# Performance work log

Measured on AMD Instinct MI355X. Metric: run time of the kernel, lower is better.

## Reference

```python
import jax, jax.numpy as jnp
import numpy as np

T, H, I, E = 8192, 1024, 2816, 8


def setup_inputs() -> dict:
    key = jax.random.key(0)
    ks = jax.random.split(key, 4)
    x = jax.random.normal(ks[0], (T, H), dtype=jnp.float32)
    router_logits = jax.random.normal(ks[1], (T, E), dtype=jnp.float32)
    # params scaled like trained weights
    w13 = jax.random.normal(ks[2], (E, 2 * I, H), dtype=jnp.float32) * (1.0 / np.sqrt(H))
    w2 = jax.random.normal(ks[3], (E, H, I), dtype=jnp.float32) * (1.0 / np.sqrt(I))
    return {"x": x, "router_logits": router_logits, "w13": w13, "w2": w2, "top_k": 2}


def reference(x, router_logits, w13, w2, top_k):
    """select_experts (softmax scoring, top-k, renormalize) + fused_experts (SiLU-gated MLP per expert, weighted combine)."""
    Ttok, Hd = x.shape
    Ex, twoI, _ = w13.shape
    Id = twoI // 2
    # --- router: softmax -> top_k -> renormalize ---
    probs = jax.nn.softmax(router_logits.astype(jnp.float32), axis=-1)  # [T, E]
    topk_w, topk_ids = jax.lax.top_k(probs, top_k)                      # [T, k]
    topk_w = topk_w / jnp.sum(topk_w, axis=-1, keepdims=True)
    # per-expert combine weight matrix [T, E] (scatter of topk weights)
    comb = jnp.zeros((Ttok, Ex), dtype=x.dtype).at[
        jnp.arange(Ttok)[:, None], topk_ids
    ].add(topk_w.astype(x.dtype))
    # --- expert MLPs: out = sum_e comb[:,e] * (silu(x W1_e^T) * (x W3_e^T)) W2_e^T ---
    out = jnp.zeros_like(x)
    for e in range(Ex):  # small fixed expert count
        gate = x @ w13[e, :Id].T          # [T, I]
        up = x @ w13[e, Id:].T            # [T, I]
        h = jax.nn.silu(gate) * up        # [T, I]
        out = out + comb[:, e:e + 1] * (h @ w2[e].T)  # [T, H]
    return out
```

## Files before the change

kernel.cpp:

```cpp
#include <hip/hip_runtime.h>
#include <hip/hip_bf16.h>

#define T_TOK 8192
#define H_DIM 1024
#define I_DIM 2816
#define E_NUM 8
#define R_TOT (2 * T_TOK)

typedef __hip_bfloat16 bf16;
typedef __attribute__((ext_vector_type(8))) short short8;
typedef __attribute__((ext_vector_type(4))) float floatx4;

__device__ inline unsigned short f2b(float f) {
    bf16 b = __float2bfloat16(f);
    unsigned short u;
    __builtin_memcpy(&u, &b, 2);
    return u;
}

__device__ inline short8 ld_cvt8(const float* p) {
    float4 f0 = *(const float4*)p;
    float4 f1 = *(const float4*)(p + 4);
    short8 r;
    r[0] = (short)f2b(f0.x); r[1] = (short)f2b(f0.y);
    r[2] = (short)f2b(f0.z); r[3] = (short)f2b(f0.w);
    r[4] = (short)f2b(f1.x); r[5] = (short)f2b(f1.y);
    r[6] = (short)f2b(f1.z); r[7] = (short)f2b(f1.w);
    return r;
}

__device__ inline void gl_lds16(const void* g, void* l) {
    __builtin_amdgcn_global_load_lds(
        (const __attribute__((address_space(1))) void*)g,
        (__attribute__((address_space(3))) void*)l, 16, 0, 0);
}


__global__ __launch_bounds__(256) void cvt_bf16_kernel(const float* __restrict__ in,
                                                       bf16* __restrict__ out, int n8) {
    int stride = gridDim.x * blockDim.x;
    for (int i = blockIdx.x * blockDim.x + threadIdx.x; i < n8; i += stride) {
        short8 v = ld_cvt8(in + (size_t)i * 8);
        *(short8*)(out + (size_t)i * 8) = v;
    }
}


__global__ void zero_counts_kernel(int* counts) {
    if (threadIdx.x < E_NUM) counts[threadIdx.x] = 0;
}

__global__ void zero_out_kernel(float* __restrict__ out) {
    size_t i = ((size_t)blockIdx.x * 256 + threadIdx.x) * 4;
    float4 z = {0.0f, 0.0f, 0.0f, 0.0f};
    *(float4*)(out + i) = z;
}

__global__ void router_kernel(const float* __restrict__ logits,
                              int* __restrict__ topk_id,
                              float* __restrict__ topk_w,
                              int* __restrict__ counts) {
    int t = blockIdx.x * blockDim.x + threadIdx.x;
    if (t >= T_TOK) return;
    float l[E_NUM];
#pragma unroll
    for (int e = 0; e < E_NUM; e++) l[e] = logits[t * E_NUM + e];
    int i0 = 0;
#pragma unroll
    for (int e = 1; e < E_NUM; e++)
        if (l[e] > l[i0]) i0 = e;
    int i1 = (i0 == 0) ? 1 : 0;
#pragma unroll
    for (int e = 0; e < E_NUM; e++) {
        if (e == i0 || e == i1) continue;
        if (l[e] > l[i1]) i1 = e;
    }
    float p1 = __expf(l[i1] - l[i0]);
    float w0 = 1.0f / (1.0f + p1);
    float w1 = p1 / (1.0f + p1);
    topk_id[2 * t] = i0;
    topk_id[2 * t + 1] = i1;
    topk_w[2 * t] = w0;
    topk_w[2 * t + 1] = w1;
    atomicAdd(&counts[i0], 1);
    atomicAdd(&counts[i1], 1);
}

__global__ void offsets_kernel(const int* __restrict__ counts,
                               int* __restrict__ offs,
                               int* __restrict__ cursor) {
    if (threadIdx.x == 0 && blockIdx.x == 0) {
        int acc = 0;
        for (int e = 0; e < E_NUM; e++) {
            offs[e] = acc;
            cursor[e] = acc;
            acc += counts[e];
        }
        offs[E_NUM] = acc;
    }
}

__global__ void scatter_kernel(const int* __restrict__ topk_id,
                               const float* __restrict__ topk_w,
                               int* __restrict__ cursor,
                               int* __restrict__ rowtok,
                               float* __restrict__ wrow) {
    int t = blockIdx.x * blockDim.x + threadIdx.x;
    if (t >= T_TOK) return;
#pragma unroll
    for (int j = 0; j < 2; j++) {
        int e = topk_id[2 * t + j];
        int r = atomicAdd(&cursor[e], 1);
        rowtok[r] = t;
        wrow[r] = topk_w[2 * t + j];
    }
}


__global__ __launch_bounds__(256) void gemm1_bf16_kernel(
    const bf16* __restrict__ xb, const bf16* __restrict__ wptr,
    long long wstride, int e_base,
    const int* __restrict__ offs, const int* __restrict__ rowtok,
    bf16* __restrict__ h) {
    const int ei = blockIdx.y >> 6;
    const int e = e_base + ei;
    const int tm = blockIdx.y & 63;
    const int mBeg = offs[e], mEnd = offs[e + 1];
    const int m0 = mBeg + tm * 128;
    if (m0 >= mEnd) return;
    const int n0 = blockIdx.x * 128;

    __shared__ alignas(16) bf16 As[128 * 32];
    __shared__ alignas(16) bf16 Bg[128 * 32];
    __shared__ alignas(16) bf16 Bu[128 * 32];

    const int tid = threadIdx.x;
    const int lane = tid & 63;
    const int wv = tid >> 6;
    const int wr = wv >> 1, wc = wv & 1;

    const int c0 = tid, c1 = tid + 256;
    const int ar0 = c0 >> 2, ks0 = (c0 & 3) * 8;
    const int ar1 = c1 >> 2, ks1 = (c1 & 3) * 8;
    const bf16* aG0 = xb + (size_t)rowtok[min(m0 + ar0, R_TOT - 1)] * H_DIM + ks0;
    const bf16* aG1 = xb + (size_t)rowtok[min(m0 + ar1, R_TOT - 1)] * H_DIM + ks1;
    const bf16* w13e = wptr + (size_t)ei * wstride;
    const bf16* bG0 = w13e + (size_t)(n0 + ar0) * H_DIM + ks0;
    const bf16* bG1 = w13e + (size_t)(n0 + ar1) * H_DIM + ks1;
    const bf16* uG0 = w13e + (size_t)(I_DIM + n0 + ar0) * H_DIM + ks0;
    const bf16* uG1 = w13e + (size_t)(I_DIM + n0 + ar1) * H_DIM + ks1;

    const int wb = wv * 64;
    bf16* dA0 = As + (size_t)wb * 8;
    bf16* dA1 = As + (size_t)(wb + 256) * 8;
    bf16* dG0 = Bg + (size_t)wb * 8;
    bf16* dG1 = Bg + (size_t)(wb + 256) * 8;
    bf16* dU0 = Bu + (size_t)wb * 8;
    bf16* dU1 = Bu + (size_t)(wb + 256) * 8;

    floatx4 accG[4][4] = {};
    floatx4 accU[4][4] = {};

    const int lr = lane & 15;
    const int kg = lane >> 4;

    for (int kt = 0; kt < H_DIM; kt += 32) {
        gl_lds16(aG0 + kt, dA0);
        gl_lds16(aG1 + kt, dA1);
        gl_lds16(bG0 + kt, dG0);
        gl_lds16(bG1 + kt, dG1);
        gl_lds16(uG0 + kt, dU0);
        gl_lds16(uG1 + kt, dU1);
        __syncthreads();

        short8 af[4], bgf[4], buf2[4];
#pragma unroll
        for (int i = 0; i < 4; i++)
            af[i] = *(const short8*)(As + (wr * 64 + i * 16 + lr) * 32 + kg * 8);
#pragma unroll
        for (int j = 0; j < 4; j++) {
            bgf[j] = *(const short8*)(Bg + (wc * 64 + j * 16 + lr) * 32 + kg * 8);
            buf2[j] = *(const short8*)(Bu + (wc * 64 + j * 16 + lr) * 32 + kg * 8);
        }
#pragma unroll
        for (int i = 0; i < 4; i++)
#pragma unroll
            for (int j = 0; j < 4; j++) {
                accG[i][j] = __builtin_amdgcn_mfma_f32_16x16x32_bf16(af[i], bgf[j], accG[i][j], 0, 0, 0);
                accU[i][j] = __builtin_amdgcn_mfma_f32_16x16x32_bf16(af[i], buf2[j], accU[i][j], 0, 0, 0);
            }
        __syncthreads();
    }

    const int quad = lane >> 4;
#pragma unroll
    for (int i = 0; i < 4; i++) {
        const int grb = m0 + wr * 64 + i * 16 + quad * 4;
#pragma unroll
        for (int j = 0; j < 4; j++) {
            const int gc = n0 + wc * 64 + j * 16 + lr;
#pragma unroll
            for (int v = 0; v < 4; v++) {
                const int gr = grb + v;
                if (gr < mEnd) {
                    float g = accG[i][j][v];
                    float u = accU[i][j][v];
                    float s = g / (1.0f + __expf(-g));
                    h[(size_t)gr * I_DIM + gc] = __float2bfloat16(s * u);
                }
            }
        }
    }
}


__global__ __launch_bounds__(256) void gemm2_bf16_kernel(
    const bf16* __restrict__ hbuf, const bf16* __restrict__ wptr,
    long long wstride, int e_base,
    const int* __restrict__ offs, const int* __restrict__ rowtok,
    const float* __restrict__ wrow, float* __restrict__ out) {
    const int ei = blockIdx.y >> 6;
    const int e = e_base + ei;
    const int tm = blockIdx.y & 63;
    const int mBeg = offs[e], mEnd = offs[e + 1];
    const int m0 = mBeg + tm * 128;
    if (m0 >= mEnd) return;
    const int n0 = blockIdx.x * 128;

    __shared__ alignas(16) bf16 As[128 * 32];
    __shared__ alignas(16) bf16 Bs[128 * 32];

    const int tid = threadIdx.x;
    const int lane = tid & 63;
    const int wv = tid >> 6;
    const int wr = wv >> 1, wc = wv & 1;

    const int c0 = tid, c1 = tid + 256;
    const int ar0 = c0 >> 2, ks0 = (c0 & 3) * 8;
    const int ar1 = c1 >> 2, ks1 = (c1 & 3) * 8;
    const bf16* aG0 = hbuf + (size_t)min(m0 + ar0, R_TOT - 1) * I_DIM + ks0;
    const bf16* aG1 = hbuf + (size_t)min(m0 + ar1, R_TOT - 1) * I_DIM + ks1;
    const bf16* w2e = wptr + (size_t)ei * wstride;
    const bf16* bG0 = w2e + (size_t)(n0 + ar0) * I_DIM + ks0;
    const bf16* bG1 = w2e + (size_t)(n0 + ar1) * I_DIM + ks1;

    const int wb = wv * 64;
    bf16* dA0 = As + (size_t)wb * 8;
    bf16* dA1 = As + (size_t)(wb + 256) * 8;
    bf16* dB0 = Bs + (size_t)wb * 8;
    bf16* dB1 = Bs + (size_t)(wb + 256) * 8;

    floatx4 acc[4][4] = {};
    const int lr = lane & 15;
    const int kg = lane >> 4;

    for (int kt = 0; kt < I_DIM; kt += 32) {
        gl_lds16(aG0 + kt, dA0);
        gl_lds16(aG1 + kt, dA1);
        gl_lds16(bG0 + kt, dB0);
        gl_lds16(bG1 + kt, dB1);
        __syncthreads();

        short8 af[4], bf_[4];
#pragma unroll
        for (int i = 0; i < 4; i++)
            af[i] = *(const short8*)(As + (wr * 64 + i * 16 + lr) * 32 + kg * 8);
#pragma unroll
        for (int j = 0; j < 4; j++)
            bf_[j] = *(const short8*)(Bs + (wc * 64 + j * 16 + lr) * 32 + kg * 8);
#pragma unroll
        for (int i = 0; i < 4; i++)
#pragma unroll
            for (int j = 0; j < 4; j++)
                acc[i][j] = __builtin_amdgcn_mfma_f32_16x16x32_bf16(af[i], bf_[j], acc[i][j], 0, 0, 0);
        __syncthreads();
    }

    const int quad = lane >> 4;
#pragma unroll
    for (int i = 0; i < 4; i++) {
        const int grb = m0 + wr * 64 + i * 16 + quad * 4;
#pragma unroll
        for (int j = 0; j < 4; j++) {
            const int gc = n0 + wc * 64 + j * 16 + lr;
#pragma unroll
            for (int v = 0; v < 4; v++) {
                const int gr = grb + v;
                if (gr < mEnd) {
                    const int t = rowtok[gr];
                    atomicAdd(&out[(size_t)t * H_DIM + gc], wrow[gr] * acc[i][j][v]);
                }
            }
        }
    }
}


__global__ __launch_bounds__(256) void gemm1_f32_kernel(
    const float* __restrict__ x, const float* __restrict__ w13,
    const int* __restrict__ offs, const int* __restrict__ rowtok,
    bf16* __restrict__ h) {
    const int e = blockIdx.y >> 6;
    const int tm = blockIdx.y & 63;
    const int mBeg = offs[e], mEnd = offs[e + 1];
    const int m0 = mBeg + tm * 128;
    if (m0 >= mEnd) return;
    const int n0 = blockIdx.x * 128;

    __shared__ alignas(16) bf16 As[128 * 32];
    __shared__ alignas(16) bf16 Bg[128 * 32];
    __shared__ alignas(16) bf16 Bu[128 * 32];

    const int tid = threadIdx.x;
    const int lane = tid & 63;
    const int wv = tid >> 6;
    const int wr = wv >> 1, wc = wv & 1;

    const int c0 = tid, c1 = tid + 256;
    const int ar0 = c0 >> 2, ks0 = (c0 & 3) * 8;
    const int ar1 = c1 >> 2, ks1 = (c1 & 3) * 8;
    const int rr0 = min(m0 + ar0, R_TOT - 1);
    const int rr1 = min(m0 + ar1, R_TOT - 1);
    const float* aG0 = x + (size_t)rowtok[rr0] * H_DIM + ks0;
    const float* aG1 = x + (size_t)rowtok[rr1] * H_DIM + ks1;
    const float* w13e = w13 + (size_t)e * (2 * I_DIM) * H_DIM;
    const float* bG0 = w13e + (size_t)(n0 + ar0) * H_DIM + ks0;
    const float* bG1 = w13e + (size_t)(n0 + ar1) * H_DIM + ks1;
    const float* uG0 = w13e + (size_t)(I_DIM + n0 + ar0) * H_DIM + ks0;
    const float* uG1 = w13e + (size_t)(I_DIM + n0 + ar1) * H_DIM + ks1;

    floatx4 accG[4][4] = {};
    floatx4 accU[4][4] = {};

    const int lr = lane & 15;
    const int kg = lane >> 4;

    for (int kt = 0; kt < H_DIM; kt += 32) {
        short8 va0 = ld_cvt8(aG0 + kt);
        short8 va1 = ld_cvt8(aG1 + kt);
        short8 vg0 = ld_cvt8(bG0 + kt);
        short8 vg1 = ld_cvt8(bG1 + kt);
        short8 vu0 = ld_cvt8(uG0 + kt);
        short8 vu1 = ld_cvt8(uG1 + kt);
        __syncthreads();
        *(short8*)(As + c0 * 8) = va0;
        *(short8*)(As + c1 * 8) = va1;
        *(short8*)(Bg + c0 * 8) = vg0;
        *(short8*)(Bg + c1 * 8) = vg1;
        *(short8*)(Bu + c0 * 8) = vu0;
        *(short8*)(Bu + c1 * 8) = vu1;
        __syncthreads();

        short8 af[4], bgf[4], buf2[4];
#pragma unroll
        for (int i = 0; i < 4; i++)
            af[i] = *(const short8*)(As + (wr * 64 + i * 16 + lr) * 32 + kg * 8);
#pragma unroll
        for (int j = 0; j < 4; j++) {
            bgf[j] = *(const short8*)(Bg + (wc * 64 + j * 16 + lr) * 32 + kg * 8);
            buf2[j] = *(const short8*)(Bu + (wc * 64 + j * 16 + lr) * 32 + kg * 8);
        }
#pragma unroll
        for (int i = 0; i < 4; i++)
#pragma unroll
            for (int j = 0; j < 4; j++) {
                accG[i][j] = __builtin_amdgcn_mfma_f32_16x16x32_bf16(af[i], bgf[j], accG[i][j], 0, 0, 0);
                accU[i][j] = __builtin_amdgcn_mfma_f32_16x16x32_bf16(af[i], buf2[j], accU[i][j], 0, 0, 0);
            }
    }

    const int quad = lane >> 4;
#pragma unroll
    for (int i = 0; i < 4; i++) {
        const int grb = m0 + wr * 64 + i * 16 + quad * 4;
#pragma unroll
        for (int j = 0; j < 4; j++) {
            const int gc = n0 + wc * 64 + j * 16 + lr;
#pragma unroll
            for (int v = 0; v < 4; v++) {
                const int gr = grb + v;
                if (gr < mEnd) {
                    float g = accG[i][j][v];
                    float u = accU[i][j][v];
                    float s = g / (1.0f + __expf(-g));
                    h[(size_t)gr * I_DIM + gc] = __float2bfloat16(s * u);
                }
            }
        }
    }
}

__global__ __launch_bounds__(256) void gemm2_f32_kernel(
    const bf16* __restrict__ hbuf, const float* __restrict__ w2,
    const int* __restrict__ offs, const int* __restrict__ rowtok,
    const float* __restrict__ wrow, float* __restrict__ out) {
    const int e = blockIdx.y >> 6;
    const int tm = blockIdx.y & 63;
    const int mBeg = offs[e], mEnd = offs[e + 1];
    const int m0 = mBeg + tm * 128;
    if (m0 >= mEnd) return;
    const int n0 = blockIdx.x * 128;

    __shared__ alignas(16) bf16 As[128 * 32];
    __shared__ alignas(16) bf16 Bs[128 * 32];

    const int tid = threadIdx.x;
    const int lane = tid & 63;
    const int wv = tid >> 6;
    const int wr = wv >> 1, wc = wv & 1;

    const int c0 = tid, c1 = tid + 256;
    const int ar0 = c0 >> 2, ks0 = (c0 & 3) * 8;
    const int ar1 = c1 >> 2, ks1 = (c1 & 3) * 8;
    const bf16* aG0 = hbuf + (size_t)min(m0 + ar0, R_TOT - 1) * I_DIM + ks0;
    const bf16* aG1 = hbuf + (size_t)min(m0 + ar1, R_TOT - 1) * I_DIM + ks1;
    const float* w2e = w2 + (size_t)e * H_DIM * I_DIM;
    const float* bG0 = w2e + (size_t)(n0 + ar0) * I_DIM + ks0;
    const float* bG1 = w2e + (size_t)(n0 + ar1) * I_DIM + ks1;

    floatx4 acc[4][4] = {};
    const int lr = lane & 15;
    const int kg = lane >> 4;

    for (int kt = 0; kt < I_DIM; kt += 32) {
        short8 va0 = *(const short8*)(aG0 + kt);
        short8 va1 = *(const short8*)(aG1 + kt);
        short8 vb0 = ld_cvt8(bG0 + kt);
        short8 vb1 = ld_cvt8(bG1 + kt);
        __syncthreads();
        *(short8*)(As + c0 * 8) = va0;
        *(short8*)(As + c1 * 8) = va1;
        *(short8*)(Bs + c0 * 8) = vb0;
        *(short8*)(Bs + c1 * 8) = vb1;
        __syncthreads();

        short8 af[4], bf_[4];
#pragma unroll
        for (int i = 0; i < 4; i++)
            af[i] = *(const short8*)(As + (wr * 64 + i * 16 + lr) * 32 + kg * 8);
#pragma unroll
        for (int j = 0; j < 4; j++)
            bf_[j] = *(const short8*)(Bs + (wc * 64 + j * 16 + lr) * 32 + kg * 8);
#pragma unroll
        for (int i = 0; i < 4; i++)
#pragma unroll
            for (int j = 0; j < 4; j++)
                acc[i][j] = __builtin_amdgcn_mfma_f32_16x16x32_bf16(af[i], bf_[j], acc[i][j], 0, 0, 0);
    }

    const int quad = lane >> 4;
#pragma unroll
    for (int i = 0; i < 4; i++) {
        const int grb = m0 + wr * 64 + i * 16 + quad * 4;
#pragma unroll
        for (int j = 0; j < 4; j++) {
            const int gc = n0 + wc * 64 + j * 16 + lr;
#pragma unroll
            for (int v = 0; v < 4; v++) {
                const int gr = grb + v;
                if (gr < mEnd) {
                    const int t = rowtok[gr];
                    atomicAdd(&out[(size_t)t * H_DIM + gc], wrow[gr] * acc[i][j][v]);
                }
            }
        }
    }
}


extern "C" void kernel_launch(void* const* d_in, const int* in_sizes, int n_in,
                              void* d_out, int out_size, void* d_ws, size_t ws_size,
                              hipStream_t stream) {
    const float* x = (const float*)d_in[0];
    const float* rl = (const float*)d_in[1];
    const float* w13 = (const float*)d_in[2];
    const float* w2 = (const float*)d_in[3];
    float* out = (float*)d_out;

    char* ws = (char*)d_ws;
    int* counts = (int*)(ws);
    int* offs = (int*)(ws + 256);
    int* cursor = (int*)(ws + 512);
    int* topk_id = (int*)(ws + 1024);
    float* topk_w = (float*)(ws + 1024 + 65536);
    int* rowtok = (int*)(ws + 1024 + 2 * 65536);
    float* wrow = (float*)(ws + 1024 + 3 * 65536);

    const size_t BASE = 1024 + 4 * 65536;
    const size_t H_BYTES = (size_t)R_TOT * I_DIM * 2;
    const size_t XB_BYTES = (size_t)T_TOK * H_DIM * 2;
    const size_t W13_BYTES = (size_t)E_NUM * 2 * I_DIM * H_DIM * 2;
    const size_t W13_SLICE = (size_t)2 * I_DIM * H_DIM * 2;
    const size_t W2_SLICE = (size_t)H_DIM * I_DIM * 2;

    bf16* h = (bf16*)(ws + BASE);
    bf16* xb = (bf16*)(ws + BASE + H_BYTES);
    bf16* wbuf = (bf16*)(ws + BASE + H_BYTES + XB_BYTES);

    const size_t NEED_BULK = BASE + H_BYTES + XB_BYTES + W13_BYTES;
    const size_t NEED_SLICE = BASE + H_BYTES + XB_BYTES + W13_SLICE;

    zero_out_kernel<<<(T_TOK * H_DIM) / (256 * 4), 256, 0, stream>>>(out);
    zero_counts_kernel<<<1, 64, 0, stream>>>(counts);
    router_kernel<<<(T_TOK + 255) / 256, 256, 0, stream>>>(rl, topk_id, topk_w, counts);
    offsets_kernel<<<1, 64, 0, stream>>>(counts, offs, cursor);
    scatter_kernel<<<(T_TOK + 255) / 256, 256, 0, stream>>>(topk_id, topk_w, cursor, rowtok, wrow);

    if (ws_size >= NEED_BULK) {
        cvt_bf16_kernel<<<2048, 256, 0, stream>>>(x, xb, (T_TOK * H_DIM) / 8);
        cvt_bf16_kernel<<<2048, 256, 0, stream>>>(w13, wbuf, (int)(W13_BYTES / 2 / 8));
        gemm1_bf16_kernel<<<dim3(I_DIM / 128, E_NUM * 64), 256, 0, stream>>>(
            xb, wbuf, (long long)2 * I_DIM * H_DIM, 0, offs, rowtok, h);
        cvt_bf16_kernel<<<2048, 256, 0, stream>>>(w2, wbuf, (E_NUM * H_DIM * I_DIM) / 8);
        gemm2_bf16_kernel<<<dim3(H_DIM / 128, E_NUM * 64), 256, 0, stream>>>(
            h, wbuf, (long long)H_DIM * I_DIM, 0, offs, rowtok, wrow, out);
    } else if (ws_size >= NEED_SLICE) {
        cvt_bf16_kernel<<<2048, 256, 0, stream>>>(x, xb, (T_TOK * H_DIM) / 8);
        for (int e = 0; e < E_NUM; e++) {
            cvt_bf16_kernel<<<1024, 256, 0, stream>>>(
                w13 + (size_t)e * 2 * I_DIM * H_DIM, wbuf, (int)(W13_SLICE / 2 / 8));
            gemm1_bf16_kernel<<<dim3(I_DIM / 128, 64), 256, 0, stream>>>(
                xb, wbuf, 0LL, e, offs, rowtok, h);
        }
        for (int e = 0; e < E_NUM; e++) {
            cvt_bf16_kernel<<<1024, 256, 0, stream>>>(
                w2 + (size_t)e * H_DIM * I_DIM, wbuf, (int)(W2_SLICE / 2 / 8));
            gemm2_bf16_kernel<<<dim3(H_DIM / 128, 64), 256, 0, stream>>>(
                h, wbuf, 0LL, e, offs, rowtok, wrow, out);
        }
    } else {
        gemm1_f32_kernel<<<dim3(I_DIM / 128, E_NUM * 64), 256, 0, stream>>>(
            x, w13, offs, rowtok, h);
        gemm2_f32_kernel<<<dim3(H_DIM / 128, E_NUM * 64), 256, 0, stream>>>(
            h, w2, offs, rowtok, wrow, out);
    }
}
```

Measured before the change: 1.184 ms.

## Double-buffer LDS tiles in both expert GEMMs to overlap loads with MFMA

Both grouped GEMM kernels now keep two LDS buffers per operand and prefetch the next K tile with direct global-to-LDS loads while MFMAs run on the current tile. This drops one barrier per iteration and is meant to hide global memory latency. Launch bounds also request three blocks per CU. The extra LDS (48 KB for gemm1) and the occupancy hint may limit residency or force register spills. Correctness relies on the barrier at the end of each iteration also covering completion of the async LDS writes.

Result: slower. 1.846 ms (+55.9%).

```diff
diff --git a/kernel.cpp b/kernel.cpp
--- a/kernel.cpp
+++ b/kernel.cpp
@@ -117,7 +117,7 @@
 }
 
 
-__global__ __launch_bounds__(256) void gemm1_bf16_kernel(
+__global__ __launch_bounds__(256, 3) void gemm1_bf16_kernel(
     const bf16* __restrict__ xb, const bf16* __restrict__ wptr,
     long long wstride, int e_base,
     const int* __restrict__ offs, const int* __restrict__ rowtok,
@@ -130,9 +130,9 @@
     if (m0 >= mEnd) return;
     const int n0 = blockIdx.x * 128;
 
-    __shared__ alignas(16) bf16 As[128 * 32];
-    __shared__ alignas(16) bf16 Bg[128 * 32];
-    __shared__ alignas(16) bf16 Bu[128 * 32];
+    __shared__ alignas(16) bf16 As[2][128 * 32];
+    __shared__ alignas(16) bf16 Bg[2][128 * 32];
+    __shared__ alignas(16) bf16 Bu[2][128 * 32];
 
     const int tid = threadIdx.x;
     const int lane = tid & 63;
@@ -150,13 +150,16 @@
     const bf16* uG0 = w13e + (size_t)(I_DIM + n0 + ar0) * H_DIM + ks0;
     const bf16* uG1 = w13e + (size_t)(I_DIM + n0 + ar1) * H_DIM + ks1;
 
-    const int wb = wv * 64;
-    bf16* dA0 = As + (size_t)wb * 8;
-    bf16* dA1 = As + (size_t)(wb + 256) * 8;
-    bf16* dG0 = Bg + (size_t)wb * 8;
-    bf16* dG1 = Bg + (size_t)(wb + 256) * 8;
-    bf16* dU0 = Bu + (size_t)wb * 8;
-    bf16* dU1 = Bu + (size_t)(wb + 256) * 8;
+    const int wb8 = (wv * 64) * 8;
+    const int wb8b = (wv * 64 + 256) * 8;
+
+#define STG1(B, KT)                          \
+    gl_lds16(aG0 + (KT), &As[B][wb8]);       \
+    gl_lds16(aG1 + (KT), &As[B][wb8b]);      \
+    gl_lds16(bG0 + (KT), &Bg[B][wb8]);       \
+    gl_lds16(bG1 + (KT), &Bg[B][wb8b]);      \
+    gl_lds16(uG0 + (KT), &Bu[B][wb8]);       \
+    gl_lds16(uG1 + (KT), &Bu[B][wb8b]);
 
     floatx4 accG[4][4] = {};
     floatx4 accU[4][4] = {};
@@ -164,23 +167,21 @@
     const int lr = lane & 15;
     const int kg = lane >> 4;
 
+    STG1(0, 0);
+    __syncthreads();
+
+    int cur = 0;
     for (int kt = 0; kt < H_DIM; kt += 32) {
-        gl_lds16(aG0 + kt, dA0);
-        gl_lds16(aG1 + kt, dA1);
-        gl_lds16(bG0 + kt, dG0);
-        gl_lds16(bG1 + kt, dG1);
-        gl_lds16(uG0 + kt, dU0);
-        gl_lds16(uG1 + kt, dU1);
-        __syncthreads();
+        if (kt + 32 < H_DIM) { STG1(cur ^ 1, kt + 32); }
 
         short8 af[4], bgf[4], buf2[4];
 #pragma unroll
         for (int i = 0; i < 4; i++)
-            af[i] = *(const short8*)(As + (wr * 64 + i * 16 + lr) * 32 + kg * 8);
+            af[i] = *(const short8*)(&As[cur][(wr * 64 + i * 16 + lr) * 32 + kg * 8]);
 #pragma unroll
         for (int j = 0; j < 4; j++) {
-            bgf[j] = *(const short8*)(Bg + (wc * 64 + j * 16 + lr) * 32 + kg * 8);
-            buf2[j] = *(const short8*)(Bu + (wc * 64 + j * 16 + lr) * 32 + kg * 8);
+            bgf[j] = *(const short8*)(&Bg[cur][(wc * 64 + j * 16 + lr) * 32 + kg * 8]);
+            buf2[j] = *(const short8*)(&Bu[cur][(wc * 64 + j * 16 + lr) * 32 + kg * 8]);
         }
 #pragma unroll
         for (int i = 0; i < 4; i++)
@@ -190,7 +191,9 @@
                 accU[i][j] = __builtin_amdgcn_mfma_f32_16x16x32_bf16(af[i], buf2[j], accU[i][j], 0, 0, 0);
             }
         __syncthreads();
-    }
+        cur ^= 1;
+    }
+#undef STG1
 
     const int quad = lane >> 4;
 #pragma unroll
@@ -214,7 +217,7 @@
 }
 
 
-__global__ __launch_bounds__(256) void gemm2_bf16_kernel(
+__global__ __launch_bounds__(256, 3) void gemm2_bf16_kernel(
     const bf16* __restrict__ hbuf, const bf16* __restrict__ wptr,
     long long wstride, int e_base,
     const int* __restrict__ offs, const int* __restrict__ rowtok,
@@ -227,8 +230,8 @@
     if (m0 >= mEnd) return;
     const int n0 = blockIdx.x * 128;
 
-    __shared__ alignas(16) bf16 As[128 * 32];
-    __shared__ alignas(16) bf16 Bs[128 * 32];
+    __shared__ alignas(16) bf16 As[2][128 * 32];
+    __shared__ alignas(16) bf16 Bs[2][128 * 32];
 
     const int tid = threadIdx.x;
     const int lane = tid & 63;
@@ -244,37 +247,42 @@
     const bf16* bG0 = w2e + (size_t)(n0 + ar0) * I_DIM + ks0;
     const bf16* bG1 = w2e + (size_t)(n0 + ar1) * I_DIM + ks1;
 
-    const int wb = wv * 64;
-    bf16* dA0 = As + (size_t)wb * 8;
-    bf16* dA1 = As + (size_t)(wb + 256) * 8;
-    bf16* dB0 = Bs + (size_t)wb * 8;
-    bf16* dB1 = Bs + (size_t)(wb + 256) * 8;
+    const int wb8 = (wv * 64) * 8;
+    const int wb8b = (wv * 64 + 256) * 8;
+
+#define STG2(B, KT)                          \
+    gl_lds16(aG0 + (KT), &As[B][wb8]);       \
+    gl_lds16(aG1 + (KT), &As[B][wb8b]);      \
+    gl_lds16(bG0 + (KT), &Bs[B][wb8]);       \
+    gl_lds16(bG1 + (KT), &Bs[B][wb8b]);
 
     floatx4 acc[4][4] = {};
     const int lr = lane & 15;
     const int kg = lane >> 4;
 
+    STG2(0, 0);
+    __syncthreads();
+
+    int cur = 0;
     for (int kt = 0; kt < I_DIM; kt += 32) {
-        gl_lds16(aG0 + kt, dA0);
-        gl_lds16(aG1 + kt, dA1);
-        gl_lds16(bG0 + kt, dB0);
-        gl_lds16(bG1 + kt, dB1);
-        __syncthreads();
+        if (kt + 32 < I_DIM) { STG2(cur ^ 1, kt + 32); }
 
         short8 af[4], bf_[4];
 #pragma unroll
         for (int i = 0; i < 4; i++)
-            af[i] = *(const short8*)(As + (wr * 64 + i * 16 + lr) * 32 + kg * 8);
+            af[i] = *(const short8*)(&As[cur][(wr * 64 + i * 16 + lr) * 32 + kg * 8]);
 #pragma unroll
         for (int j = 0; j < 4; j++)
-            bf_[j] = *(const short8*)(Bs + (wc * 64 + j * 16 + lr) * 32 + kg * 8);
+            bf_[j] = *(const short8*)(&Bs[cur][(wc * 64 + j * 16 + lr) * 32 + kg * 8]);
 #pragma unroll
         for (int i = 0; i < 4; i++)
 #pragma unroll
             for (int j = 0; j < 4; j++)
                 acc[i][j] = __builtin_amdgcn_mfma_f32_16x16x32_bf16(af[i], bf_[j], acc[i][j], 0, 0, 0);
         __syncthreads();
-    }
+        cur ^= 1;
+    }
+#undef STG2
 
     const int quad = lane >> 4;
 #pragma unroll
```
